# Optimization experiments

Measured on AMD Instinct MI355X. Metric: run time of the kernel, lower is better.

The kernel has to match this reference:

```python
import jax, jax.numpy as jnp
import numpy as np

TOP_K = 2

def setup_inputs() -> dict:
    key = jax.random.key(0)
    k1, k2 = jax.random.split(key)
    x = jax.random.normal(k1, (8192, 4096), dtype=jnp.float32)
    # nn.Linear(n_input, n_experts, bias=False): weight [n_experts, n_input]
    W = jax.random.normal(k2, (64, 4096), dtype=jnp.float32) * (1.0 / np.sqrt(4096))
    return {"x": x, "W": W}

def reference(x, W):
    logits = jnp.einsum('td,ed->te', x, W)            # [tokens, n_experts]
    probs = jax.nn.softmax(logits, axis=-1)
    top_w, top_i = jax.lax.top_k(probs, TOP_K)        # [tokens, k]
    rows = jnp.arange(probs.shape[0])[:, None]
    weights = jnp.zeros_like(probs).at[rows, top_i].set(top_w)
    return weights, top_i
```

## Files before the change

### kernel.cpp

```cpp
#include <hip/hip_runtime.h>
#include <math.h>


#define TOKENS 8192
#define DIM    4096
#define NEXP   64
#define NCHW   (DIM / 32)
#define FRAGS  ((size_t)NCHW * 4 * 64 * 8)

#define KS     8
#define KSEG   (DIM / KS)
#define NCH    (KSEG / 32)

#define SBAR() __builtin_amdgcn_sched_barrier(0)

typedef __attribute__((ext_vector_type(8))) short  short8;
typedef __attribute__((ext_vector_type(4))) float  f32x4;
typedef __attribute__((ext_vector_type(8))) float  f32x8;

__device__ __forceinline__ void bf16split(float v, short& hi, short& lo) {
    unsigned u = __float_as_uint(v);
    hi = (short)(u >> 16);
    float r = v - __uint_as_float(u & 0xffff0000u);
    lo = (short)(__float_as_uint(r) >> 16);
}

__global__ void tg_prepw(const float* __restrict__ W,
                         short* __restrict__ Whf, short* __restrict__ Wlf) {
    int gid  = blockIdx.x * 256 + threadIdx.x;
    int c    = gid >> 8, rem = gid & 255;
    int nt   = rem >> 6, lane = rem & 63;
    int e    = nt * 16 + (lane & 15);
    int kb   = c * 32 + (lane >> 4) * 8;
    const float* wp = W + (size_t)e * DIM + kb;
    short8 h, l;
#pragma unroll
    for (int j = 0; j < 8; ++j) {
        short hh, ll;
        bf16split(wp[j], hh, ll);
        h[j] = hh; l[j] = ll;
    }
    size_t o = ((size_t)(c * 4 + nt) * 64 + lane) * 8;
    *reinterpret_cast<short8*>(Whf + o) = h;
    *reinterpret_cast<short8*>(Wlf + o) = l;
}

__global__ __launch_bounds__(512, 2)
void tg_mfma(const float* __restrict__ x,
             const short* __restrict__ Whf, const short* __restrict__ Wlf,
             float* __restrict__ part) {
    __shared__ short8 Bls[2][NCH][256];

    const int tid  = threadIdx.x;
    const int lane = tid & 63;
    const int wave = tid >> 6;
    const int tg   = blockIdx.x >> 3;
    const int ks   = blockIdx.x & 7;
    const int t0   = tg * 128 + wave * 16;
    const int row  = lane & 15;
    const int grp  = lane >> 4;

    {
        const short8* srch = reinterpret_cast<const short8*>(Whf) + (size_t)ks * (NCH * 256);
        const short8* srcl = reinterpret_cast<const short8*>(Wlf) + (size_t)ks * (NCH * 256);
        short8* d0 = &Bls[0][0][0];
        short8* d1 = &Bls[1][0][0];
#pragma unroll
        for (int i = 0; i < 8; ++i) {
            d0[i * 512 + tid] = srch[i * 512 + tid];
            d1[i * 512 + tid] = srcl[i * 512 + tid];
        }
    }
    __syncthreads();

    const float* xp = x + (size_t)(t0 + row) * DIM + ks * KSEG + grp * 8;

    f32x4 acc[4];
#pragma unroll
    for (int nt = 0; nt < 4; ++nt) acc[nt] = (f32x4){0.f, 0.f, 0.f, 0.f};

    short8 bA[8], bB[8];
    auto dsB = [&](short8 (&b)[8], int c) {
#pragma unroll
        for (int nt = 0; nt < 4; ++nt) {
            b[nt]     = Bls[0][c][nt * 64 + lane];
            b[4 + nt] = Bls[1][c][nt * 64 + lane];
        }
    };
    auto ldx = [&](int c) {
        return *reinterpret_cast<const f32x8*>(xp + c * 32);
    };
    auto cvt = [&](const f32x8& xv, short8& ah, short8& al) {
#pragma unroll
        for (int j = 0; j < 8; ++j) {
            short hh, ll;
            bf16split(xv[j], hh, ll);
            ah[j] = hh; al[j] = ll;
        }
    };
    auto mfma12 = [&](const short8& ah, const short8& al, const short8 (&b)[8]) {
#pragma unroll
        for (int nt = 0; nt < 4; ++nt)
            acc[nt] = __builtin_amdgcn_mfma_f32_16x16x32_bf16(ah, b[nt], acc[nt], 0, 0, 0);
#pragma unroll
        for (int nt = 0; nt < 4; ++nt)
            acc[nt] = __builtin_amdgcn_mfma_f32_16x16x32_bf16(al, b[nt], acc[nt], 0, 0, 0);
#pragma unroll
        for (int nt = 0; nt < 4; ++nt)
            acc[nt] = __builtin_amdgcn_mfma_f32_16x16x32_bf16(ah, b[4 + nt], acc[nt], 0, 0, 0);
    };

    f32x8 x0 = ldx(0), x1 = ldx(1), x2 = ldx(2),
          x3 = ldx(3), x4 = ldx(4), x5 = ldx(5);
    dsB(bA, 0);
    SBAR();

    short8 ah, al;
#define PH(c, XV, BC, BN)                                            \
    {                                                                \
        cvt(XV, ah, al);                \
        SBAR();                                                      \
        if ((c) + 1 < NCH) dsB(BN, (c) + 1);                         \
        if ((c) + 6 < NCH) XV = ldx((c) + 6);                        \
        SBAR();                                                      \
        mfma12(ah, al, BC);                                          \
        SBAR();                                                      \
    }

    PH(0,  x0, bA, bB)
    PH(1,  x1, bB, bA)
    PH(2,  x2, bA, bB)
    PH(3,  x3, bB, bA)
    PH(4,  x4, bA, bB)
    PH(5,  x5, bB, bA)
    PH(6,  x0, bA, bB)
    PH(7,  x1, bB, bA)
    PH(8,  x2, bA, bB)
    PH(9,  x3, bB, bA)
    PH(10, x4, bA, bB)
    PH(11, x5, bB, bA)
    PH(12, x0, bA, bB)
    PH(13, x1, bB, bA)
    PH(14, x2, bA, bB)
    PH(15, x3, bB, bA)
#undef PH

    float* pp = part + ((size_t)ks * TOKENS + t0) * NEXP;
#pragma unroll
    for (int nt = 0; nt < 4; ++nt)
#pragma unroll
        for (int r = 0; r < 4; ++r)
            pp[(grp * 4 + r) * NEXP + nt * 16 + row] = acc[nt][r];
}

__global__ __launch_bounds__(256)
void tg_final(const float* __restrict__ part,
              float* __restrict__ out_w, float* __restrict__ out_i) {
    const int lane = threadIdx.x & 63;
    const int wv   = threadIdx.x >> 6;
    const int t    = blockIdx.x * 4 + wv;

    float s = 0.0f;
#pragma unroll
    for (int k = 0; k < KS; ++k)
        s += part[((size_t)k * TOKENS + t) * NEXP + lane];

    float m = s;
#pragma unroll
    for (int o = 32; o > 0; o >>= 1) m = fmaxf(m, __shfl_xor(m, o));
    float p = expf(s - m);
    float sum = p;
#pragma unroll
    for (int o = 32; o > 0; o >>= 1) sum += __shfl_xor(sum, o);
    const float prob = p / sum;

    float v1 = prob; int i1 = lane;
#pragma unroll
    for (int o = 32; o > 0; o >>= 1) {
        float ov = __shfl_xor(v1, o); int oi = __shfl_xor(i1, o);
        if (ov > v1 || (ov == v1 && oi < i1)) { v1 = ov; i1 = oi; }
    }
    float v2 = (lane == i1) ? -1.0f : prob; int i2 = lane;
#pragma unroll
    for (int o = 32; o > 0; o >>= 1) {
        float ov = __shfl_xor(v2, o); int oi = __shfl_xor(i2, o);
        if (ov > v2 || (ov == v2 && oi < i2)) { v2 = ov; i2 = oi; }
    }

    out_w[(size_t)t * NEXP + lane] = (lane == i1) ? v1 : (lane == i2) ? v2 : 0.0f;
    if (lane == 0) {
        out_i[(size_t)t * 2 + 0] = (float)i1;
        out_i[(size_t)t * 2 + 1] = (float)i2;
    }
}

extern "C" void kernel_launch(void* const* d_in, const int* in_sizes, int n_in,
                              void* d_out, int out_size, void* d_ws, size_t ws_size,
                              hipStream_t stream) {
    const float* x = (const float*)d_in[0];
    const float* W = (const float*)d_in[1];
    float* out_w = (float*)d_out;
    float* out_i = out_w + (size_t)TOKENS * NEXP;

    float* part = (float*)d_ws;
    short* Whf  = (short*)((char*)d_ws + (size_t)KS * TOKENS * NEXP * 4);
    short* Wlf  = Whf + FRAGS;

    tg_prepw<<<dim3(128), dim3(256), 0, stream>>>(W, Whf, Wlf);
    tg_mfma <<<dim3(64 * KS), dim3(512), 0, stream>>>(x, Whf, Wlf, part);
    tg_final<<<dim3(TOKENS / 4), dim3(256), 0, stream>>>(part, out_w, out_i);
}
```

Measured before the change: 43.79 us.

## Switch router GEMM to 32x32x16 MFMA with 32-token waves

Replaces the 16x16x32 bf16 MFMA tiles with 32x32x16 tiles, so each wave covers 32 tokens and all 64 experts with two 16-wide accumulators. The W fragment layout in the prep kernel and the LDS layout are reordered to match the new operand format, and the per-lane x prefetch is reshaped to three two-half chunks. This is meant to cut LDS B-fragment reads and instruction count per FLOP. The trade-off is that the grid is halved to 256 blocks, leaving fewer waves per CU to hide the latency of the large fp32 x stream.

```diff
diff --git a/kernel.cpp b/kernel.cpp
--- a/kernel.cpp
+++ b/kernel.cpp
@@ -14,9 +14,9 @@
 
 #define SBAR() __builtin_amdgcn_sched_barrier(0)
 
-typedef __attribute__((ext_vector_type(8))) short  short8;
-typedef __attribute__((ext_vector_type(4))) float  f32x4;
-typedef __attribute__((ext_vector_type(8))) float  f32x8;
+typedef __attribute__((ext_vector_type(8)))  short short8;
+typedef __attribute__((ext_vector_type(8)))  float f32x8;
+typedef __attribute__((ext_vector_type(16))) float f32x16;
 
 __device__ __forceinline__ void bf16split(float v, short& hi, short& lo) {
     unsigned u = __float_as_uint(v);
@@ -29,9 +29,10 @@
                          short* __restrict__ Whf, short* __restrict__ Wlf) {
     int gid  = blockIdx.x * 256 + threadIdx.x;
     int c    = gid >> 8, rem = gid & 255;
-    int nt   = rem >> 6, lane = rem & 63;
-    int e    = nt * 16 + (lane & 15);
-    int kb   = c * 32 + (lane >> 4) * 8;
+    int f    = rem >> 6, lane = rem & 63;
+    int ks2  = f >> 1, nt = f & 1;
+    int e    = nt * 32 + (lane & 31);
+    int kb   = c * 32 + ks2 * 16 + (lane >> 5) * 8;
     const float* wp = W + (size_t)e * DIM + kb;
     short8 h, l;
 #pragma unroll
@@ -40,7 +41,7 @@
         bf16split(wp[j], hh, ll);
         h[j] = hh; l[j] = ll;
     }
-    size_t o = ((size_t)(c * 4 + nt) * 64 + lane) * 8;
+    size_t o = ((size_t)(c * 4 + f) * 64 + lane) * 8;
     *reinterpret_cast<short8*>(Whf + o) = h;
     *reinterpret_cast<short8*>(Wlf + o) = l;
 }
@@ -49,22 +50,22 @@
 void tg_mfma(const float* __restrict__ x,
              const short* __restrict__ Whf, const short* __restrict__ Wlf,
              float* __restrict__ part) {
-    __shared__ short8 Bls[2][NCH][256];
+    __shared__ short8 Bls[2][NCH][4][64];
 
     const int tid  = threadIdx.x;
     const int lane = tid & 63;
     const int wave = tid >> 6;
     const int tg   = blockIdx.x >> 3;
     const int ks   = blockIdx.x & 7;
-    const int t0   = tg * 128 + wave * 16;
-    const int row  = lane & 15;
-    const int grp  = lane >> 4;
+    const int t0   = tg * 256 + wave * 32;
+    const int r32  = lane & 31;
+    const int grp  = lane >> 5;
 
     {
-        const short8* srch = reinterpret_cast<const short8*>(Whf) + (size_t)ks * (NCH * 256);
-        const short8* srcl = reinterpret_cast<const short8*>(Wlf) + (size_t)ks * (NCH * 256);
-        short8* d0 = &Bls[0][0][0];
-        short8* d1 = &Bls[1][0][0];
+        const short8* srch = reinterpret_cast<const short8*>(Whf) + (size_t)ks * (NCH * 4 * 64);
+        const short8* srcl = reinterpret_cast<const short8*>(Wlf) + (size_t)ks * (NCH * 4 * 64);
+        short8* d0 = &Bls[0][0][0][0];
+        short8* d1 = &Bls[1][0][0][0];
 #pragma unroll
         for (int i = 0; i < 8; ++i) {
             d0[i * 512 + tid] = srch[i * 512 + tid];
@@ -73,22 +74,21 @@
     }
     __syncthreads();
 
-    const float* xp = x + (size_t)(t0 + row) * DIM + ks * KSEG + grp * 8;
-
-    f32x4 acc[4];
-#pragma unroll
-    for (int nt = 0; nt < 4; ++nt) acc[nt] = (f32x4){0.f, 0.f, 0.f, 0.f};
+    const float* xp = x + (size_t)(t0 + r32) * DIM + ks * KSEG + grp * 8;
+
+    f32x16 acc0 = {0,0,0,0,0,0,0,0,0,0,0,0,0,0,0,0};
+    f32x16 acc1 = {0,0,0,0,0,0,0,0,0,0,0,0,0,0,0,0};
 
     short8 bA[8], bB[8];
     auto dsB = [&](short8 (&b)[8], int c) {
 #pragma unroll
-        for (int nt = 0; nt < 4; ++nt) {
-            b[nt]     = Bls[0][c][nt * 64 + lane];
-            b[4 + nt] = Bls[1][c][nt * 64 + lane];
+        for (int f = 0; f < 4; ++f) {
+            b[f]     = Bls[0][c][f][lane];
+            b[4 + f] = Bls[1][c][f][lane];
         }
     };
-    auto ldx = [&](int c) {
-        return *reinterpret_cast<const f32x8*>(xp + c * 32);
+    auto ldx = [&](int c, int h) {
+        return *reinterpret_cast<const f32x8*>(xp + c * 32 + h * 16);
     };
     auto cvt = [&](const f32x8& xv, short8& ah, short8& al) {
 #pragma unroll
@@ -98,59 +98,65 @@
             ah[j] = hh; al[j] = ll;
         }
     };
-    auto mfma12 = [&](const short8& ah, const short8& al, const short8 (&b)[8]) {
-#pragma unroll
-        for (int nt = 0; nt < 4; ++nt)
-            acc[nt] = __builtin_amdgcn_mfma_f32_16x16x32_bf16(ah, b[nt], acc[nt], 0, 0, 0);
-#pragma unroll
-        for (int nt = 0; nt < 4; ++nt)
-            acc[nt] = __builtin_amdgcn_mfma_f32_16x16x32_bf16(al, b[nt], acc[nt], 0, 0, 0);
-#pragma unroll
-        for (int nt = 0; nt < 4; ++nt)
-            acc[nt] = __builtin_amdgcn_mfma_f32_16x16x32_bf16(ah, b[4 + nt], acc[nt], 0, 0, 0);
-    };
-
-    f32x8 x0 = ldx(0), x1 = ldx(1), x2 = ldx(2),
-          x3 = ldx(3), x4 = ldx(4), x5 = ldx(5);
+    auto mfma12 = [&](const short8& ah0, const short8& al0,
+                      const short8& ah1, const short8& al1, const short8 (&b)[8]) {
+        acc0 = __builtin_amdgcn_mfma_f32_32x32x16_bf16(ah0, b[0], acc0, 0, 0, 0);
+        acc1 = __builtin_amdgcn_mfma_f32_32x32x16_bf16(ah0, b[1], acc1, 0, 0, 0);
+        acc0 = __builtin_amdgcn_mfma_f32_32x32x16_bf16(ah1, b[2], acc0, 0, 0, 0);
+        acc1 = __builtin_amdgcn_mfma_f32_32x32x16_bf16(ah1, b[3], acc1, 0, 0, 0);
+        acc0 = __builtin_amdgcn_mfma_f32_32x32x16_bf16(al0, b[0], acc0, 0, 0, 0);
+        acc1 = __builtin_amdgcn_mfma_f32_32x32x16_bf16(al0, b[1], acc1, 0, 0, 0);
+        acc0 = __builtin_amdgcn_mfma_f32_32x32x16_bf16(al1, b[2], acc0, 0, 0, 0);
+        acc1 = __builtin_amdgcn_mfma_f32_32x32x16_bf16(al1, b[3], acc1, 0, 0, 0);
+        acc0 = __builtin_amdgcn_mfma_f32_32x32x16_bf16(ah0, b[4], acc0, 0, 0, 0);
+        acc1 = __builtin_amdgcn_mfma_f32_32x32x16_bf16(ah0, b[5], acc1, 0, 0, 0);
+        acc0 = __builtin_amdgcn_mfma_f32_32x32x16_bf16(ah1, b[6], acc0, 0, 0, 0);
+        acc1 = __builtin_amdgcn_mfma_f32_32x32x16_bf16(ah1, b[7], acc1, 0, 0, 0);
+    };
+
+    f32x8 xA0 = ldx(0, 0), xA1 = ldx(0, 1);
+    f32x8 xB0 = ldx(1, 0), xB1 = ldx(1, 1);
+    f32x8 xC0 = ldx(2, 0), xC1 = ldx(2, 1);
     dsB(bA, 0);
     SBAR();
 
-    short8 ah, al;
-#define PH(c, XV, BC, BN)                                            \
+    short8 ah0, al0, ah1, al1;
+#define PH(c, XV0, XV1, BC, BN)                                      \
     {                                                                \
-        cvt(XV, ah, al);                \
+        cvt(XV0, ah0, al0); cvt(XV1, ah1, al1);                      \
         SBAR();                                                      \
         if ((c) + 1 < NCH) dsB(BN, (c) + 1);                         \
-        if ((c) + 6 < NCH) XV = ldx((c) + 6);                        \
+        if ((c) + 3 < NCH) { XV0 = ldx((c) + 3, 0); XV1 = ldx((c) + 3, 1); } \
         SBAR();                                                      \
-        mfma12(ah, al, BC);                                          \
+        mfma12(ah0, al0, ah1, al1, BC);                              \
         SBAR();                                                      \
     }
 
-    PH(0,  x0, bA, bB)
-    PH(1,  x1, bB, bA)
-    PH(2,  x2, bA, bB)
-    PH(3,  x3, bB, bA)
-    PH(4,  x4, bA, bB)
-    PH(5,  x5, bB, bA)
-    PH(6,  x0, bA, bB)
-    PH(7,  x1, bB, bA)
-    PH(8,  x2, bA, bB)
-    PH(9,  x3, bB, bA)
-    PH(10, x4, bA, bB)
-    PH(11, x5, bB, bA)
-    PH(12, x0, bA, bB)
-    PH(13, x1, bB, bA)
-    PH(14, x2, bA, bB)
-    PH(15, x3, bB, bA)
+    PH(0,  xA0, xA1, bA, bB)
+    PH(1,  xB0, xB1, bB, bA)
+    PH(2,  xC0, xC1, bA, bB)
+    PH(3,  xA0, xA1, bB, bA)
+    PH(4,  xB0, xB1, bA, bB)
+    PH(5,  xC0, xC1, bB, bA)
+    PH(6,  xA0, xA1, bA, bB)
+    PH(7,  xB0, xB1, bB, bA)
+    PH(8,  xC0, xC1, bA, bB)
+    PH(9,  xA0, xA1, bB, bA)
+    PH(10, xB0, xB1, bA, bB)
+    PH(11, xC0, xC1, bB, bA)
+    PH(12, xA0, xA1, bA, bB)
+    PH(13, xB0, xB1, bB, bA)
+    PH(14, xC0, xC1, bA, bB)
+    PH(15, xA0, xA1, bB, bA)
 #undef PH
 
     float* pp = part + ((size_t)ks * TOKENS + t0) * NEXP;
 #pragma unroll
-    for (int nt = 0; nt < 4; ++nt)
-#pragma unroll
-        for (int r = 0; r < 4; ++r)
-            pp[(grp * 4 + r) * NEXP + nt * 16 + row] = acc[nt][r];
+    for (int r = 0; r < 16; ++r) {
+        const int rr = (r & 3) + 8 * (r >> 2) + 4 * grp;
+        pp[rr * NEXP + r32]      = acc0[r];
+        pp[rr * NEXP + 32 + r32] = acc1[r];
+    }
 }
 
 __global__ __launch_bounds__(256)
@@ -207,6 +213,6 @@
     short* Wlf  = Whf + FRAGS;
 
     tg_prepw<<<dim3(128), dim3(256), 0, stream>>>(W, Whf, Wlf);
-    tg_mfma <<<dim3(64 * KS), dim3(512), 0, stream>>>(x, Whf, Wlf, part);
+    tg_mfma <<<dim3((TOKENS / 256) * KS), dim3(512), 0, stream>>>(x, Whf, Wlf, part);
     tg_final<<<dim3(TOKENS / 4), dim3(256), 0, stream>>>(part, out_w, out_i);
 }
```

Result: slower. 47.91 us (+9.4%).

## Fuse W bf16 split into GEMM kernel and use 1024-thread blocks

Applied to the files above, without the earlier changes.

Drops the separate weight-preparation kernel. Each GEMM block now loads its fp32 W slice, splits it into bf16 hi/lo parts and writes them straight into shared memory. Blocks grow to 1024 threads covering 256 tokens, which halves the grid, and the launch bounds change to (1024, 4). This removes one kernel launch and the workspace round trip for the weights. In exchange, every block repeats the W conversion, and the tighter launch bound may cap the register budget and cause spills.

```diff
diff --git a/kernel.cpp b/kernel.cpp
--- a/kernel.cpp
+++ b/kernel.cpp
@@ -5,8 +5,6 @@
 #define TOKENS 8192
 #define DIM    4096
 #define NEXP   64
-#define NCHW   (DIM / 32)
-#define FRAGS  ((size_t)NCHW * 4 * 64 * 8)
 
 #define KS     8
 #define KSEG   (DIM / KS)
@@ -25,51 +23,39 @@
     lo = (short)(__float_as_uint(r) >> 16);
 }
 
-__global__ void tg_prepw(const float* __restrict__ W,
-                         short* __restrict__ Whf, short* __restrict__ Wlf) {
-    int gid  = blockIdx.x * 256 + threadIdx.x;
-    int c    = gid >> 8, rem = gid & 255;
-    int nt   = rem >> 6, lane = rem & 63;
-    int e    = nt * 16 + (lane & 15);
-    int kb   = c * 32 + (lane >> 4) * 8;
-    const float* wp = W + (size_t)e * DIM + kb;
-    short8 h, l;
-#pragma unroll
-    for (int j = 0; j < 8; ++j) {
-        short hh, ll;
-        bf16split(wp[j], hh, ll);
-        h[j] = hh; l[j] = ll;
-    }
-    size_t o = ((size_t)(c * 4 + nt) * 64 + lane) * 8;
-    *reinterpret_cast<short8*>(Whf + o) = h;
-    *reinterpret_cast<short8*>(Wlf + o) = l;
-}
-
-__global__ __launch_bounds__(512, 2)
-void tg_mfma(const float* __restrict__ x,
-             const short* __restrict__ Whf, const short* __restrict__ Wlf,
+__global__ __launch_bounds__(1024, 4)
+void tg_mfma(const float* __restrict__ x, const float* __restrict__ W,
              float* __restrict__ part) {
-    __shared__ short8 Bls[2][NCH][256];
+    __shared__ short8 Bls[2][NCH][4][64];
 
     const int tid  = threadIdx.x;
     const int lane = tid & 63;
     const int wave = tid >> 6;
     const int tg   = blockIdx.x >> 3;
     const int ks   = blockIdx.x & 7;
-    const int t0   = tg * 128 + wave * 16;
+    const int t0   = tg * 256 + wave * 16;
     const int row  = lane & 15;
     const int grp  = lane >> 4;
 
-    {
-        const short8* srch = reinterpret_cast<const short8*>(Whf) + (size_t)ks * (NCH * 256);
-        const short8* srcl = reinterpret_cast<const short8*>(Wlf) + (size_t)ks * (NCH * 256);
-        short8* d0 = &Bls[0][0][0];
-        short8* d1 = &Bls[1][0][0];
 #pragma unroll
-        for (int i = 0; i < 8; ++i) {
-            d0[i * 512 + tid] = srch[i * 512 + tid];
-            d1[i * 512 + tid] = srcl[i * 512 + tid];
+    for (int s4 = 0; s4 < 4; ++s4) {
+        const int s   = s4 * 1024 + tid;
+        const int c   = s >> 8;
+        const int rem = s & 255;
+        const int nt  = rem >> 6;
+        const int ln  = rem & 63;
+        const int e   = nt * 16 + (ln & 15);
+        const int kb  = ks * KSEG + c * 32 + (ln >> 4) * 8;
+        const f32x8 wv = *reinterpret_cast<const f32x8*>(W + (size_t)e * DIM + kb);
+        short8 h, l;
+#pragma unroll
+        for (int j = 0; j < 8; ++j) {
+            short hh, ll;
+            bf16split(wv[j], hh, ll);
+            h[j] = hh; l[j] = ll;
         }
+        Bls[0][c][nt][ln] = h;
+        Bls[1][c][nt][ln] = l;
     }
     __syncthreads();
 
@@ -83,8 +69,8 @@
     auto dsB = [&](short8 (&b)[8], int c) {
 #pragma unroll
         for (int nt = 0; nt < 4; ++nt) {
-            b[nt]     = Bls[0][c][nt * 64 + lane];
-            b[4 + nt] = Bls[1][c][nt * 64 + lane];
+            b[nt]     = Bls[0][c][nt][lane];
+            b[4 + nt] = Bls[1][c][nt][lane];
         }
     };
     auto ldx = [&](int c) {
@@ -203,10 +189,7 @@
     float* out_i = out_w + (size_t)TOKENS * NEXP;
 
     float* part = (float*)d_ws;
-    short* Whf  = (short*)((char*)d_ws + (size_t)KS * TOKENS * NEXP * 4);
-    short* Wlf  = Whf + FRAGS;
 
-    tg_prepw<<<dim3(128), dim3(256), 0, stream>>>(W, Whf, Wlf);
-    tg_mfma <<<dim3(64 * KS), dim3(512), 0, stream>>>(x, Whf, Wlf, part);
+    tg_mfma <<<dim3((TOKENS / 256) * KS), dim3(1024), 0, stream>>>(x, W, part);
     tg_final<<<dim3(TOKENS / 4), dim3(256), 0, stream>>>(part, out_w, out_i);
 }
```

Result: slower. 68.38 us (+56.2%).
